# Kernel optimization log

Hardware: AMD Instinct MI355X
Metric: run time of the kernel (lower is better)

The kernel has to match this reference:

```python
import jax, jax.numpy as jnp
import numpy as np


def _conv1d(x, w):
    # x: (B, W, Cin), w: (K, Cin, Cout), SAME padding, stride 1
    return jax.lax.conv_general_dilated(
        x, w, window_strides=(1,), padding='SAME',
        dimension_numbers=('NWC', 'WIO', 'NWC'))


def setup_inputs() -> dict:
    key = jax.random.key(0)
    ks = jax.random.split(key, 5)
    B, T, F, C, K = 64, 64, 256, 64, 9  # batch, num_frames, frame_size(noise_size), filters, kernel
    z = jax.random.normal(ks[0], (B, T, F, 1), dtype=jnp.float32)
    h0 = jax.random.normal(ks[1], (B, F, C), dtype=jnp.float32)
    c0 = jax.random.normal(ks[2], (B, F, C), dtype=jnp.float32)
    Wx = jax.random.normal(ks[3], (K, 1, 4 * C), dtype=jnp.float32) * 0.1
    Wh = jax.random.normal(ks[4], (K, C, 4 * C), dtype=jnp.float32) * 0.1
    b = jnp.zeros((4 * C,), dtype=jnp.float32)
    return {'z': z, 'h0': h0, 'c0': c0, 'Wx': Wx, 'Wh': Wh, 'b': b}


def reference(z, h0, c0, Wx, Wh, b):
    # z: (B, T, F, 1); h0/c0: (B, F, C)
    B = z.shape[0]
    FORGET_BIAS = 1.0  # tf ConvLSTMCell default

    def step(carry, z_t):
        h, c = carry
        gates = _conv1d(z_t, Wx) + _conv1d(h, Wh) + b  # (B, F, 4C)
        i, j, f, o = jnp.split(gates, 4, axis=-1)       # tf gate order: i, new_input, f, o
        c_new = c * jax.nn.sigmoid(f + FORGET_BIAS) + jax.nn.sigmoid(i) * jnp.tanh(j)
        h_new = jnp.tanh(c_new) * jax.nn.sigmoid(o)
        # post_rnn_callback: tanh(mean over channels)
        out = jnp.tanh(jnp.mean(h_new, axis=-1))        # (B, F)
        return (h_new, c_new), out

    z_t_first = jnp.transpose(z, (1, 0, 2, 3))          # (T, B, F, 1)
    (_, _), outs = jax.lax.scan(step, (h0, c0), z_t_first)  # outs: (T, B, F)
    # concat frames along frame axis -> (B, T*F)
    return jnp.transpose(outs, (1, 0, 2)).reshape(B, -1)
```

## Files before the change

kernel.cpp:

```cpp
#include <hip/hip_runtime.h>
#include <hip/hip_bf16.h>

#define BB 64
#define TT 64
#define FF 256
#define CC 64
#define GG 256
#define HP 264
#define GST 264

using frag_ab = __attribute__((ext_vector_type(8))) short;
using f32x4   = __attribute__((ext_vector_type(4))) float;

__device__ __forceinline__ float sigmoidf_(float x) {
    return 1.0f / (1.0f + __expf(-x));
}
__device__ __forceinline__ float tanhf_(float x) {
    const float e = __expf(2.0f * x);
    return 1.0f - 2.0f / (e + 1.0f);
}
__device__ __forceinline__ void split2(float v, short* hi, short* lo) {
    __hip_bfloat16 h = __float2bfloat16(v);
    __hip_bfloat16 l = __float2bfloat16(v - __bfloat162float(h));
    *hi = *reinterpret_cast<short*>(&h);
    *lo = *reinterpret_cast<short*>(&l);
}

__global__ __launch_bounds__(256) void prep_kernel(
    const float* __restrict__ Wh, const float* __restrict__ Wx,
    const float* __restrict__ h0,
    short* __restrict__ WhPh, short* __restrict__ WhPl,
    short* __restrict__ WxTh, short* __restrict__ WxTl,
    short* __restrict__ hAh, short* __restrict__ hAl,
    short* __restrict__ hBh, short* __restrict__ hBl)
{
    const int n = blockIdx.x * 256 + threadIdx.x;
    if (n < BB * HP * CC) {
        const int c = n & 63;
        const int r = (n >> 6) % HP;
        const int b = n / (HP * CC);
        if (r < 4 || r >= 260) {
            hAh[n] = 0; hAl[n] = 0; hBh[n] = 0; hBl[n] = 0;
        } else {
            split2(h0[(b * FF + (r - 4)) * CC + c], &hAh[n], &hAl[n]);
        }
    }
    if (n < 9 * GG * CC) {
        const int c32 = n & 31;
        const int g = (n >> 5) & 255;
        const int p = n >> 13;
        const int k = p >> 1;
        const int cin = (p & 1) * 32 + c32;
        split2(Wh[(k * CC + cin) * GG + g], &WhPh[n], &WhPl[n]);
    }
    if (n < GG * 32) {
        const int kz = n & 31;
        const int g = n >> 5;
        split2(kz < 9 ? Wx[kz * GG + g] : 0.0f, &WxTh[n], &WxTl[n]);
    }
}

__global__ __launch_bounds__(512, 4) void convlstm_step(
    const float* __restrict__ z,
    const short* __restrict__ hinh, const short* __restrict__ hinl,
    const float* __restrict__ c_in,
    const short* __restrict__ WhPh, const short* __restrict__ WhPl,
    const short* __restrict__ WxTh, const short* __restrict__ WxTl,
    const float* __restrict__ bias,
    short* __restrict__ houth, short* __restrict__ houtl,
    float* __restrict__ c_out,
    float* __restrict__ out, int t)
{
    __shared__ __align__(16) char hbyh[72 * 128];
    __shared__ __align__(16) char hbyl[72 * 128];
    __shared__ __align__(16) char zbyh[64 * 64];
    __shared__ __align__(16) char zbyl[64 * 64];
    __shared__ __align__(16) float gbuf[32 * GST];

    const int b = blockIdx.x;
    const int f0 = blockIdx.y * 64;
    const int tid = threadIdx.x;
    const int lane = tid & 63;
    const int w = tid >> 6;

    for (int idx = tid; idx < 72 * 8; idx += 512) {
        const int row = idx >> 3, slot = idx & 7;
        const int off = (b * HP + f0 + row) * CC + slot * 8;
        const frag_ab vh = *reinterpret_cast<const frag_ab*>(hinh + off);
        const frag_ab vl = *reinterpret_cast<const frag_ab*>(hinl + off);
        const int a = row * 128 + ((slot ^ (row & 7)) << 4);
        *reinterpret_cast<frag_ab*>(&hbyh[a]) = vh;
        *reinterpret_cast<frag_ab*>(&hbyl[a]) = vl;
    }
    if (tid < 256) {
        const int row = tid >> 2, slot = tid & 3;
        const float* zr = z + ((long)b * TT + t) * FF;
        short vh[8], vl[8];
        #pragma unroll
        for (int j = 0; j < 8; ++j) {
            const int kz = slot * 8 + j;
            const int f = f0 + row - 4 + kz;
            const float val = (kz < 9 && f >= 0 && f < FF) ? zr[f] : 0.0f;
            split2(val, &vh[j], &vl[j]);
        }
        const int a = row * 64 + ((slot ^ (row & 3)) << 4);
        *reinterpret_cast<frag_ab*>(&zbyh[a]) = *reinterpret_cast<frag_ab*>(vh);
        *reinterpret_cast<frag_ab*>(&zbyl[a]) = *reinterpret_cast<frag_ab*>(vl);
    }
    __syncthreads();

    const int rA = lane & 15;
    const int sA = lane >> 4;
    const int gbase = w * 32;

    f32x4 acc[4][2];
    #pragma unroll
    for (int gtI = 0; gtI < 2; ++gtI) {
        const float bv = bias[gbase + gtI * 16 + rA];
        #pragma unroll
        for (int Mt = 0; Mt < 4; ++Mt) acc[Mt][gtI] = (f32x4){bv, bv, bv, bv};
    }

    const int bln = rA * 32 + sA * 8;
    frag_ab cb[4];
    {
        const int o0 = (0 * GG + gbase) * 32 + bln;
        cb[0] = *reinterpret_cast<const frag_ab*>(WhPh + o0);
        cb[1] = *reinterpret_cast<const frag_ab*>(WhPh + o0 + 16 * 32);
        cb[2] = *reinterpret_cast<const frag_ab*>(WhPl + o0);
        cb[3] = *reinterpret_cast<const frag_ab*>(WhPl + o0 + 16 * 32);
    }

    #pragma unroll
    for (int p = 0; p < 18; ++p) {
        frag_ab nb[4];
        if (p < 17) {
            const int o0 = ((p + 1) * GG + gbase) * 32 + bln;
            nb[0] = *reinterpret_cast<const frag_ab*>(WhPh + o0);
            nb[1] = *reinterpret_cast<const frag_ab*>(WhPh + o0 + 16 * 32);
            nb[2] = *reinterpret_cast<const frag_ab*>(WhPl + o0);
            nb[3] = *reinterpret_cast<const frag_ab*>(WhPl + o0 + 16 * 32);
        } else {
            const int o0 = gbase * 32 + bln;
            nb[0] = *reinterpret_cast<const frag_ab*>(WxTh + o0);
            nb[1] = *reinterpret_cast<const frag_ab*>(WxTh + o0 + 16 * 32);
            nb[2] = *reinterpret_cast<const frag_ab*>(WxTl + o0);
            nb[3] = *reinterpret_cast<const frag_ab*>(WxTl + o0 + 16 * 32);
        }
        const int k = p >> 1, kk = p & 1;
        const int sl = kk * 4 + sA;
        frag_ab ah[4], al[4];
        #pragma unroll
        for (int Mt = 0; Mt < 4; ++Mt) {
            const int r = Mt * 16 + rA + k;
            const int a = r * 128 + ((sl ^ (r & 7)) << 4);
            ah[Mt] = *reinterpret_cast<const frag_ab*>(&hbyh[a]);
            al[Mt] = *reinterpret_cast<const frag_ab*>(&hbyl[a]);
        }
        #pragma unroll
        for (int Mt = 0; Mt < 4; ++Mt) {
            acc[Mt][0] = __builtin_amdgcn_mfma_f32_16x16x32_bf16(ah[Mt], cb[0], acc[Mt][0], 0, 0, 0);
            acc[Mt][1] = __builtin_amdgcn_mfma_f32_16x16x32_bf16(ah[Mt], cb[1], acc[Mt][1], 0, 0, 0);
        }
        #pragma unroll
        for (int Mt = 0; Mt < 4; ++Mt) {
            acc[Mt][0] = __builtin_amdgcn_mfma_f32_16x16x32_bf16(ah[Mt], cb[2], acc[Mt][0], 0, 0, 0);
            acc[Mt][1] = __builtin_amdgcn_mfma_f32_16x16x32_bf16(ah[Mt], cb[3], acc[Mt][1], 0, 0, 0);
        }
        #pragma unroll
        for (int Mt = 0; Mt < 4; ++Mt) {
            acc[Mt][0] = __builtin_amdgcn_mfma_f32_16x16x32_bf16(al[Mt], cb[0], acc[Mt][0], 0, 0, 0);
            acc[Mt][1] = __builtin_amdgcn_mfma_f32_16x16x32_bf16(al[Mt], cb[1], acc[Mt][1], 0, 0, 0);
        }
        cb[0] = nb[0]; cb[1] = nb[1]; cb[2] = nb[2]; cb[3] = nb[3];
    }
    {
        frag_ab ah[4], al[4];
        #pragma unroll
        for (int Mt = 0; Mt < 4; ++Mt) {
            const int r = Mt * 16 + rA;
            const int a = r * 64 + ((sA ^ (r & 3)) << 4);
            ah[Mt] = *reinterpret_cast<const frag_ab*>(&zbyh[a]);
            al[Mt] = *reinterpret_cast<const frag_ab*>(&zbyl[a]);
        }
        #pragma unroll
        for (int Mt = 0; Mt < 4; ++Mt) {
            acc[Mt][0] = __builtin_amdgcn_mfma_f32_16x16x32_bf16(ah[Mt], cb[0], acc[Mt][0], 0, 0, 0);
            acc[Mt][1] = __builtin_amdgcn_mfma_f32_16x16x32_bf16(ah[Mt], cb[1], acc[Mt][1], 0, 0, 0);
            acc[Mt][0] = __builtin_amdgcn_mfma_f32_16x16x32_bf16(ah[Mt], cb[2], acc[Mt][0], 0, 0, 0);
            acc[Mt][1] = __builtin_amdgcn_mfma_f32_16x16x32_bf16(ah[Mt], cb[3], acc[Mt][1], 0, 0, 0);
            acc[Mt][0] = __builtin_amdgcn_mfma_f32_16x16x32_bf16(al[Mt], cb[0], acc[Mt][0], 0, 0, 0);
            acc[Mt][1] = __builtin_amdgcn_mfma_f32_16x16x32_bf16(al[Mt], cb[1], acc[Mt][1], 0, 0, 0);
        }
    }

    #pragma unroll
    for (int pass = 0; pass < 2; ++pass) {
        if (pass) __syncthreads();
        #pragma unroll
        for (int Mh = 0; Mh < 2; ++Mh) {
            const int Mt = pass * 2 + Mh;
            #pragma unroll
            for (int gtI = 0; gtI < 2; ++gtI) {
                const int g = gbase + gtI * 16 + rA;
                float* gp = &gbuf[(Mh * 16 + sA * 4) * GST + g];
                gp[0]       = acc[Mt][gtI][0];
                gp[GST]     = acc[Mt][gtI][1];
                gp[2 * GST] = acc[Mt][gtI][2];
                gp[3 * GST] = acc[Mt][gtI][3];
            }
        }
        __syncthreads();

        const int fl = tid >> 4;
        const int ch0 = (tid & 15) * 4;
        const int frow = pass * 32 + fl;
        const int f = f0 + frow;
        const float* gr = &gbuf[fl * GST];
        const f32x4 gi = *reinterpret_cast<const f32x4*>(gr + ch0);
        const f32x4 gj = *reinterpret_cast<const f32x4*>(gr + 64 + ch0);
        const f32x4 gf = *reinterpret_cast<const f32x4*>(gr + 128 + ch0);
        const f32x4 go = *reinterpret_cast<const f32x4*>(gr + 192 + ch0);

        const int cix = (b * FF + f) * CC + ch0;
        const float4 cold = *reinterpret_cast<const float4*>(&c_in[cix]);
        const float co_[4] = {cold.x, cold.y, cold.z, cold.w};

        float hsum = 0.0f;
        float cv[4];
        short hh[4], hl[4];
        #pragma unroll
        for (int j = 0; j < 4; ++j) {
            const float cnew = co_[j] * sigmoidf_(gf[j] + 1.0f) + sigmoidf_(gi[j]) * tanhf_(gj[j]);
            const float hnew = tanhf_(cnew) * sigmoidf_(go[j]);
            cv[j] = cnew;
            split2(hnew, &hh[j], &hl[j]);
            hsum += hnew;
        }
        *reinterpret_cast<float4*>(&c_out[cix]) = make_float4(cv[0], cv[1], cv[2], cv[3]);
        const int hix = (b * HP + 4 + f) * CC + ch0;
        *reinterpret_cast<uint2*>(&houth[hix]) = *reinterpret_cast<uint2*>(hh);
        *reinterpret_cast<uint2*>(&houtl[hix]) = *reinterpret_cast<uint2*>(hl);

        hsum += __shfl_xor(hsum, 1);
        hsum += __shfl_xor(hsum, 2);
        hsum += __shfl_xor(hsum, 4);
        hsum += __shfl_xor(hsum, 8);
        if ((tid & 15) == 0)
            out[(long)b * (TT * FF) + t * FF + f] = tanhf_(hsum * (1.0f / 64.0f));
    }
}

extern "C" void kernel_launch(void* const* d_in, const int* in_sizes, int n_in,
                              void* d_out, int out_size, void* d_ws, size_t ws_size,
                              hipStream_t stream) {
    const float* z    = (const float*)d_in[0];
    const float* h0   = (const float*)d_in[1];
    const float* c0   = (const float*)d_in[2];
    const float* Wx   = (const float*)d_in[3];
    const float* Wh   = (const float*)d_in[4];
    const float* bias = (const float*)d_in[5];
    float* out = (float*)d_out;

    const int SEp = BB * HP * CC;
    const int SE  = BB * FF * CC;
    short* hAh = (short*)d_ws;
    short* hAl = hAh + SEp;
    short* hBh = hAl + SEp;
    short* hBl = hBh + SEp;
    float* cW  = (float*)(hBl + SEp);
    short* WhPh = (short*)(cW + SE);
    short* WhPl = WhPh + 9 * GG * CC;
    short* WxTh = WhPl + 9 * GG * CC;
    short* WxTl = WxTh + GG * 32;

    prep_kernel<<<(SEp + 255) / 256, 256, 0, stream>>>(Wh, Wx, h0, WhPh, WhPl,
                                                       WxTh, WxTl, hAh, hAl, hBh, hBl);

    dim3 grid(BB, FF / 64);
    for (int t = 0; t < TT; ++t) {
        const short* hih = (t & 1) ? hBh : hAh;
        const short* hil = (t & 1) ? hBl : hAl;
        short* hoh = (t & 1) ? hAh : hBh;
        short* hol = (t & 1) ? hAl : hBl;
        const float* cin = (t == 0) ? c0 : cW;
        convlstm_step<<<grid, 512, 0, stream>>>(z, hih, hil, cin,
                                                WhPh, WhPl, WxTh, WxTl, bias,
                                                hoh, hol, cW, out, t);
    }
}
```

Measured before the change: 1.026 ms.

## Software-pipeline LDS A-fragment loads and prefetch c/bias/weights before staging

Restructures the MFMA main loop so the next iteration's shared-memory h fragments are loaded alongside the next weight fragments, double-buffering both A and B operands. The z-input tile is folded in as a 19th pipeline stage. The first weight fragments, the bias values and the old cell state c are issued before the LDS staging loop so their global latency overlaps with it. MFMA blocks are wrapped in s_setprio, and launch bounds are relaxed from 4 to 2 waves per SIMD so the extra live registers fit. The cost is higher register pressure and possibly lower occupancy.

```diff
diff --git a/kernel.cpp b/kernel.cpp
--- a/kernel.cpp
+++ b/kernel.cpp
@@ -60,7 +60,7 @@
     }
 }
 
-__global__ __launch_bounds__(512, 4) void convlstm_step(
+__global__ __launch_bounds__(512, 2) void convlstm_step(
     const float* __restrict__ z,
     const short* __restrict__ hinh, const short* __restrict__ hinl,
     const float* __restrict__ c_in,
@@ -83,6 +83,28 @@
     const int lane = tid & 63;
     const int w = tid >> 6;
 
+    const int rA = lane & 15;
+    const int sA = lane >> 4;
+    const int gbase = w * 32;
+    const int bln = rA * 32 + sA * 8;
+
+    frag_ab cb[4];
+    {
+        const int o0 = gbase * 32 + bln;
+        cb[0] = *reinterpret_cast<const frag_ab*>(WhPh + o0);
+        cb[1] = *reinterpret_cast<const frag_ab*>(WhPh + o0 + 512);
+        cb[2] = *reinterpret_cast<const frag_ab*>(WhPl + o0);
+        cb[3] = *reinterpret_cast<const frag_ab*>(WhPl + o0 + 512);
+    }
+    const int flE = tid >> 4;
+    const int ch0E = (tid & 15) * 4;
+    const int cixE0 = (b * FF + f0 + flE) * CC + ch0E;
+    const int cixE1 = cixE0 + 32 * CC;
+    const float4 cold0 = *reinterpret_cast<const float4*>(&c_in[cixE0]);
+    const float4 cold1 = *reinterpret_cast<const float4*>(&c_in[cixE1]);
+    const float bv0 = bias[gbase + rA];
+    const float bv1 = bias[gbase + 16 + rA];
+
     for (int idx = tid; idx < 72 * 8; idx += 512) {
         const int row = idx >> 3, slot = idx & 7;
         const int off = (b * HP + f0 + row) * CC + slot * 8;
@@ -109,88 +131,76 @@
     }
     __syncthreads();
 
-    const int rA = lane & 15;
-    const int sA = lane >> 4;
-    const int gbase = w * 32;
-
     f32x4 acc[4][2];
     #pragma unroll
-    for (int gtI = 0; gtI < 2; ++gtI) {
-        const float bv = bias[gbase + gtI * 16 + rA];
-        #pragma unroll
-        for (int Mt = 0; Mt < 4; ++Mt) acc[Mt][gtI] = (f32x4){bv, bv, bv, bv};
-    }
-
-    const int bln = rA * 32 + sA * 8;
-    frag_ab cb[4];
-    {
-        const int o0 = (0 * GG + gbase) * 32 + bln;
-        cb[0] = *reinterpret_cast<const frag_ab*>(WhPh + o0);
-        cb[1] = *reinterpret_cast<const frag_ab*>(WhPh + o0 + 16 * 32);
-        cb[2] = *reinterpret_cast<const frag_ab*>(WhPl + o0);
-        cb[3] = *reinterpret_cast<const frag_ab*>(WhPl + o0 + 16 * 32);
-    }
-
-    #pragma unroll
-    for (int p = 0; p < 18; ++p) {
-        frag_ab nb[4];
+    for (int Mt = 0; Mt < 4; ++Mt) {
+        acc[Mt][0] = (f32x4){bv0, bv0, bv0, bv0};
+        acc[Mt][1] = (f32x4){bv1, bv1, bv1, bv1};
+    }
+
+    frag_ab cah[4], cal[4];
+    #pragma unroll
+    for (int Mt = 0; Mt < 4; ++Mt) {
+        const int r = Mt * 16 + rA;
+        const int a = r * 128 + ((sA ^ (r & 7)) << 4);
+        cah[Mt] = *reinterpret_cast<const frag_ab*>(&hbyh[a]);
+        cal[Mt] = *reinterpret_cast<const frag_ab*>(&hbyl[a]);
+    }
+
+    #pragma unroll
+    for (int p = 0; p < 19; ++p) {
+        frag_ab nah[4], nal[4], nb[4];
         if (p < 17) {
-            const int o0 = ((p + 1) * GG + gbase) * 32 + bln;
+            const int pn = p + 1;
+            const int k = pn >> 1, kk = pn & 1;
+            const int sl = kk * 4 + sA;
+            #pragma unroll
+            for (int Mt = 0; Mt < 4; ++Mt) {
+                const int r = Mt * 16 + rA + k;
+                const int a = r * 128 + ((sl ^ (r & 7)) << 4);
+                nah[Mt] = *reinterpret_cast<const frag_ab*>(&hbyh[a]);
+                nal[Mt] = *reinterpret_cast<const frag_ab*>(&hbyl[a]);
+            }
+            const int o0 = (pn * GG + gbase) * 32 + bln;
             nb[0] = *reinterpret_cast<const frag_ab*>(WhPh + o0);
-            nb[1] = *reinterpret_cast<const frag_ab*>(WhPh + o0 + 16 * 32);
+            nb[1] = *reinterpret_cast<const frag_ab*>(WhPh + o0 + 512);
             nb[2] = *reinterpret_cast<const frag_ab*>(WhPl + o0);
-            nb[3] = *reinterpret_cast<const frag_ab*>(WhPl + o0 + 16 * 32);
-        } else {
+            nb[3] = *reinterpret_cast<const frag_ab*>(WhPl + o0 + 512);
+        } else if (p == 17) {
+            #pragma unroll
+            for (int Mt = 0; Mt < 4; ++Mt) {
+                const int r = Mt * 16 + rA;
+                const int a = r * 64 + ((sA ^ (r & 3)) << 4);
+                nah[Mt] = *reinterpret_cast<const frag_ab*>(&zbyh[a]);
+                nal[Mt] = *reinterpret_cast<const frag_ab*>(&zbyl[a]);
+            }
             const int o0 = gbase * 32 + bln;
             nb[0] = *reinterpret_cast<const frag_ab*>(WxTh + o0);
-            nb[1] = *reinterpret_cast<const frag_ab*>(WxTh + o0 + 16 * 32);
+            nb[1] = *reinterpret_cast<const frag_ab*>(WxTh + o0 + 512);
             nb[2] = *reinterpret_cast<const frag_ab*>(WxTl + o0);
-            nb[3] = *reinterpret_cast<const frag_ab*>(WxTl + o0 + 16 * 32);
-        }
-        const int k = p >> 1, kk = p & 1;
-        const int sl = kk * 4 + sA;
-        frag_ab ah[4], al[4];
+            nb[3] = *reinterpret_cast<const frag_ab*>(WxTl + o0 + 512);
+        }
+        __builtin_amdgcn_s_setprio(1);
         #pragma unroll
         for (int Mt = 0; Mt < 4; ++Mt) {
-            const int r = Mt * 16 + rA + k;
-            const int a = r * 128 + ((sl ^ (r & 7)) << 4);
-            ah[Mt] = *reinterpret_cast<const frag_ab*>(&hbyh[a]);
-            al[Mt] = *reinterpret_cast<const frag_ab*>(&hbyl[a]);
+            acc[Mt][0] = __builtin_amdgcn_mfma_f32_16x16x32_bf16(cah[Mt], cb[0], acc[Mt][0], 0, 0, 0);
+            acc[Mt][1] = __builtin_amdgcn_mfma_f32_16x16x32_bf16(cah[Mt], cb[1], acc[Mt][1], 0, 0, 0);
         }
         #pragma unroll
         for (int Mt = 0; Mt < 4; ++Mt) {
-            acc[Mt][0] = __builtin_amdgcn_mfma_f32_16x16x32_bf16(ah[Mt], cb[0], acc[Mt][0], 0, 0, 0);
-            acc[Mt][1] = __builtin_amdgcn_mfma_f32_16x16x32_bf16(ah[Mt], cb[1], acc[Mt][1], 0, 0, 0);
+            acc[Mt][0] = __builtin_amdgcn_mfma_f32_16x16x32_bf16(cah[Mt], cb[2], acc[Mt][0], 0, 0, 0);
+            acc[Mt][1] = __builtin_amdgcn_mfma_f32_16x16x32_bf16(cah[Mt], cb[3], acc[Mt][1], 0, 0, 0);
         }
         #pragma unroll
         for (int Mt = 0; Mt < 4; ++Mt) {
-            acc[Mt][0] = __builtin_amdgcn_mfma_f32_16x16x32_bf16(ah[Mt], cb[2], acc[Mt][0], 0, 0, 0);
-            acc[Mt][1] = __builtin_amdgcn_mfma_f32_16x16x32_bf16(ah[Mt], cb[3], acc[Mt][1], 0, 0, 0);
-        }
-        #pragma unroll
-        for (int Mt = 0; Mt < 4; ++Mt) {
-            acc[Mt][0] = __builtin_amdgcn_mfma_f32_16x16x32_bf16(al[Mt], cb[0], acc[Mt][0], 0, 0, 0);
-            acc[Mt][1] = __builtin_amdgcn_mfma_f32_16x16x32_bf16(al[Mt], cb[1], acc[Mt][1], 0, 0, 0);
-        }
-        cb[0] = nb[0]; cb[1] = nb[1]; cb[2] = nb[2]; cb[3] = nb[3];
-    }
-    {
-        frag_ab ah[4], al[4];
-        #pragma unroll
-        for (int Mt = 0; Mt < 4; ++Mt) {
-            const int r = Mt * 16 + rA;
-            const int a = r * 64 + ((sA ^ (r & 3)) << 4);
-            ah[Mt] = *reinterpret_cast<const frag_ab*>(&zbyh[a]);
-            al[Mt] = *reinterpret_cast<const frag_ab*>(&zbyl[a]);
-        }
-        #pragma unroll
-        for (int Mt = 0; Mt < 4; ++Mt) {
-            acc[Mt][0] = __builtin_amdgcn_mfma_f32_16x16x32_bf16(ah[Mt], cb[0], acc[Mt][0], 0, 0, 0);
-            acc[Mt][1] = __builtin_amdgcn_mfma_f32_16x16x32_bf16(ah[Mt], cb[1], acc[Mt][1], 0, 0, 0);
-            acc[Mt][0] = __builtin_amdgcn_mfma_f32_16x16x32_bf16(ah[Mt], cb[2], acc[Mt][0], 0, 0, 0);
-            acc[Mt][1] = __builtin_amdgcn_mfma_f32_16x16x32_bf16(ah[Mt], cb[3], acc[Mt][1], 0, 0, 0);
-            acc[Mt][0] = __builtin_amdgcn_mfma_f32_16x16x32_bf16(al[Mt], cb[0], acc[Mt][0], 0, 0, 0);
-            acc[Mt][1] = __builtin_amdgcn_mfma_f32_16x16x32_bf16(al[Mt], cb[1], acc[Mt][1], 0, 0, 0);
+            acc[Mt][0] = __builtin_amdgcn_mfma_f32_16x16x32_bf16(cal[Mt], cb[0], acc[Mt][0], 0, 0, 0);
+            acc[Mt][1] = __builtin_amdgcn_mfma_f32_16x16x32_bf16(cal[Mt], cb[1], acc[Mt][1], 0, 0, 0);
+        }
+        __builtin_amdgcn_s_setprio(0);
+        if (p < 18) {
+            #pragma unroll
+            for (int Mt = 0; Mt < 4; ++Mt) { cah[Mt] = nah[Mt]; cal[Mt] = nal[Mt]; }
+            cb[0] = nb[0]; cb[1] = nb[1]; cb[2] = nb[2]; cb[3] = nb[3];
         }
     }
 
@@ -212,18 +222,14 @@
         }
         __syncthreads();
 
-        const int fl = tid >> 4;
-        const int ch0 = (tid & 15) * 4;
-        const int frow = pass * 32 + fl;
-        const int f = f0 + frow;
-        const float* gr = &gbuf[fl * GST];
-        const f32x4 gi = *reinterpret_cast<const f32x4*>(gr + ch0);
-        const f32x4 gj = *reinterpret_cast<const f32x4*>(gr + 64 + ch0);
-        const f32x4 gf = *reinterpret_cast<const f32x4*>(gr + 128 + ch0);
-        const f32x4 go = *reinterpret_cast<const f32x4*>(gr + 192 + ch0);
-
-        const int cix = (b * FF + f) * CC + ch0;
-        const float4 cold = *reinterpret_cast<const float4*>(&c_in[cix]);
+        const int f = f0 + pass * 32 + flE;
+        const float* gr = &gbuf[flE * GST];
+        const f32x4 gi = *reinterpret_cast<const f32x4*>(gr + ch0E);
+        const f32x4 gj = *reinterpret_cast<const f32x4*>(gr + 64 + ch0E);
+        const f32x4 gf = *reinterpret_cast<const f32x4*>(gr + 128 + ch0E);
+        const f32x4 go = *reinterpret_cast<const f32x4*>(gr + 192 + ch0E);
+
+        const float4 cold = pass ? cold1 : cold0;
         const float co_[4] = {cold.x, cold.y, cold.z, cold.w};
 
         float hsum = 0.0f;
@@ -237,8 +243,9 @@
             split2(hnew, &hh[j], &hl[j]);
             hsum += hnew;
         }
+        const int cix = (b * FF + f) * CC + ch0E;
         *reinterpret_cast<float4*>(&c_out[cix]) = make_float4(cv[0], cv[1], cv[2], cv[3]);
-        const int hix = (b * HP + 4 + f) * CC + ch0;
+        const int hix = (b * HP + 4 + f) * CC + ch0E;
         *reinterpret_cast<uint2*>(&houth[hix]) = *reinterpret_cast<uint2*>(hh);
         *reinterpret_cast<uint2*>(&houtl[hix]) = *reinterpret_cast<uint2*>(hl);
 
```

Result: no change. 1.029 ms (+0.3%).

## Retile ConvLSTM step to 32-frame blocks with 256 threads and wider gate tiles

Applied to the files above, without the earlier changes.

Halves the frame tile per block (64 to 32) and threads (512 to 256), so the grid doubles to 512 blocks, and each wave now covers 64 gate columns over 2 M tiles instead of 32 columns over 4. The weight fragment loads are restructured per gate tile, c_in and bias loads are hoisted before the h staging, the z-projection is folded into the main loop, and s_setprio wraps the MFMA bursts. The epilogue becomes a single pass with 8 channels per thread, removing the second gbuf round-trip and a barrier. This aims for more parallelism per timestep and less serialization, at the cost of redundant halo loads (40 rows per 32) and more weight-fragment traffic per output.

```diff
diff --git a/kernel.cpp b/kernel.cpp
--- a/kernel.cpp
+++ b/kernel.cpp
@@ -7,7 +7,8 @@
 #define CC 64
 #define GG 256
 #define HP 264
-#define GST 264
+#define TFR 32
+#define GST 260
 
 using frag_ab = __attribute__((ext_vector_type(8))) short;
 using f32x4   = __attribute__((ext_vector_type(4))) float;
@@ -60,7 +61,7 @@
     }
 }
 
-__global__ __launch_bounds__(512, 4) void convlstm_step(
+__global__ __launch_bounds__(256, 2) void convlstm_step(
     const float* __restrict__ z,
     const short* __restrict__ hinh, const short* __restrict__ hinl,
     const float* __restrict__ c_in,
@@ -71,19 +72,41 @@
     float* __restrict__ c_out,
     float* __restrict__ out, int t)
 {
-    __shared__ __align__(16) char hbyh[72 * 128];
-    __shared__ __align__(16) char hbyl[72 * 128];
-    __shared__ __align__(16) char zbyh[64 * 64];
-    __shared__ __align__(16) char zbyl[64 * 64];
-    __shared__ __align__(16) float gbuf[32 * GST];
+    __shared__ __align__(16) char hbyh[40 * 128];
+    __shared__ __align__(16) char hbyl[40 * 128];
+    __shared__ __align__(16) char zbyh[32 * 64];
+    __shared__ __align__(16) char zbyl[32 * 64];
+    __shared__ __align__(16) float gbuf[TFR * GST];
 
     const int b = blockIdx.x;
-    const int f0 = blockIdx.y * 64;
+    const int f0 = blockIdx.y * TFR;
     const int tid = threadIdx.x;
     const int lane = tid & 63;
     const int w = tid >> 6;
 
-    for (int idx = tid; idx < 72 * 8; idx += 512) {
+    const int rA = lane & 15;
+    const int sA = lane >> 4;
+    const int gbase = w * 64;
+    const int bln = rA * 32 + sA * 8;
+
+    frag_ab cbh[4], cbl[4];
+    #pragma unroll
+    for (int gtI = 0; gtI < 4; ++gtI) {
+        const int o0 = (gbase + gtI * 16 + rA) * 32 + sA * 8;
+        cbh[gtI] = *reinterpret_cast<const frag_ab*>(WhPh + o0);
+        cbl[gtI] = *reinterpret_cast<const frag_ab*>(WhPl + o0);
+    }
+    const int flE = tid >> 3;
+    const int ch0E = (tid & 7) * 8;
+    const int cixE = (b * FF + f0 + flE) * CC + ch0E;
+    const float4 cold0 = *reinterpret_cast<const float4*>(&c_in[cixE]);
+    const float4 cold1 = *reinterpret_cast<const float4*>(&c_in[cixE + 4]);
+
+    float bv[4];
+    #pragma unroll
+    for (int gtI = 0; gtI < 4; ++gtI) bv[gtI] = bias[gbase + gtI * 16 + rA];
+
+    for (int idx = tid; idx < 40 * 8; idx += 256) {
         const int row = idx >> 3, slot = idx & 7;
         const int off = (b * HP + f0 + row) * CC + slot * 8;
         const frag_ab vh = *reinterpret_cast<const frag_ab*>(hinh + off);
@@ -92,7 +115,7 @@
         *reinterpret_cast<frag_ab*>(&hbyh[a]) = vh;
         *reinterpret_cast<frag_ab*>(&hbyl[a]) = vl;
     }
-    if (tid < 256) {
+    if (tid < 128) {
         const int row = tid >> 2, slot = tid & 3;
         const float* zr = z + ((long)b * TT + t) * FF;
         short vh[8], vl[8];
@@ -109,146 +132,117 @@
     }
     __syncthreads();
 
-    const int rA = lane & 15;
-    const int sA = lane >> 4;
-    const int gbase = w * 32;
-
-    f32x4 acc[4][2];
-    #pragma unroll
-    for (int gtI = 0; gtI < 2; ++gtI) {
-        const float bv = bias[gbase + gtI * 16 + rA];
-        #pragma unroll
-        for (int Mt = 0; Mt < 4; ++Mt) acc[Mt][gtI] = (f32x4){bv, bv, bv, bv};
-    }
-
-    const int bln = rA * 32 + sA * 8;
-    frag_ab cb[4];
-    {
-        const int o0 = (0 * GG + gbase) * 32 + bln;
-        cb[0] = *reinterpret_cast<const frag_ab*>(WhPh + o0);
-        cb[1] = *reinterpret_cast<const frag_ab*>(WhPh + o0 + 16 * 32);
-        cb[2] = *reinterpret_cast<const frag_ab*>(WhPl + o0);
-        cb[3] = *reinterpret_cast<const frag_ab*>(WhPl + o0 + 16 * 32);
-    }
-
-    #pragma unroll
-    for (int p = 0; p < 18; ++p) {
-        frag_ab nb[4];
+    f32x4 acc[2][4];
+    #pragma unroll
+    for (int Mt = 0; Mt < 2; ++Mt)
+        #pragma unroll
+        for (int gtI = 0; gtI < 4; ++gtI)
+            acc[Mt][gtI] = (f32x4){bv[gtI], bv[gtI], bv[gtI], bv[gtI]};
+
+    #pragma unroll
+    for (int p = 0; p < 19; ++p) {
+        frag_ab nbh[4], nbl[4];
         if (p < 17) {
-            const int o0 = ((p + 1) * GG + gbase) * 32 + bln;
-            nb[0] = *reinterpret_cast<const frag_ab*>(WhPh + o0);
-            nb[1] = *reinterpret_cast<const frag_ab*>(WhPh + o0 + 16 * 32);
-            nb[2] = *reinterpret_cast<const frag_ab*>(WhPl + o0);
-            nb[3] = *reinterpret_cast<const frag_ab*>(WhPl + o0 + 16 * 32);
+            #pragma unroll
+            for (int gtI = 0; gtI < 4; ++gtI) {
+                const int o0 = ((p + 1) * GG + gbase + gtI * 16 + rA) * 32 + sA * 8;
+                nbh[gtI] = *reinterpret_cast<const frag_ab*>(WhPh + o0);
+                nbl[gtI] = *reinterpret_cast<const frag_ab*>(WhPl + o0);
+            }
+        } else if (p == 17) {
+            #pragma unroll
+            for (int gtI = 0; gtI < 4; ++gtI) {
+                const int o0 = (gbase + gtI * 16 + rA) * 32 + sA * 8;
+                nbh[gtI] = *reinterpret_cast<const frag_ab*>(WxTh + o0);
+                nbl[gtI] = *reinterpret_cast<const frag_ab*>(WxTl + o0);
+            }
+        }
+        frag_ab ah[2], al[2];
+        if (p < 18) {
+            const int k = p >> 1, kk = p & 1;
+            const int sl = kk * 4 + sA;
+            #pragma unroll
+            for (int Mt = 0; Mt < 2; ++Mt) {
+                const int r = Mt * 16 + rA + k;
+                const int a = r * 128 + ((sl ^ (r & 7)) << 4);
+                ah[Mt] = *reinterpret_cast<const frag_ab*>(&hbyh[a]);
+                al[Mt] = *reinterpret_cast<const frag_ab*>(&hbyl[a]);
+            }
         } else {
-            const int o0 = gbase * 32 + bln;
-            nb[0] = *reinterpret_cast<const frag_ab*>(WxTh + o0);
-            nb[1] = *reinterpret_cast<const frag_ab*>(WxTh + o0 + 16 * 32);
-            nb[2] = *reinterpret_cast<const frag_ab*>(WxTl + o0);
-            nb[3] = *reinterpret_cast<const frag_ab*>(WxTl + o0 + 16 * 32);
-        }
-        const int k = p >> 1, kk = p & 1;
-        const int sl = kk * 4 + sA;
-        frag_ab ah[4], al[4];
-        #pragma unroll
-        for (int Mt = 0; Mt < 4; ++Mt) {
-            const int r = Mt * 16 + rA + k;
-            const int a = r * 128 + ((sl ^ (r & 7)) << 4);
-            ah[Mt] = *reinterpret_cast<const frag_ab*>(&hbyh[a]);
-            al[Mt] = *reinterpret_cast<const frag_ab*>(&hbyl[a]);
-        }
-        #pragma unroll
-        for (int Mt = 0; Mt < 4; ++Mt) {
-            acc[Mt][0] = __builtin_amdgcn_mfma_f32_16x16x32_bf16(ah[Mt], cb[0], acc[Mt][0], 0, 0, 0);
-            acc[Mt][1] = __builtin_amdgcn_mfma_f32_16x16x32_bf16(ah[Mt], cb[1], acc[Mt][1], 0, 0, 0);
-        }
-        #pragma unroll
-        for (int Mt = 0; Mt < 4; ++Mt) {
-            acc[Mt][0] = __builtin_amdgcn_mfma_f32_16x16x32_bf16(ah[Mt], cb[2], acc[Mt][0], 0, 0, 0);
-            acc[Mt][1] = __builtin_amdgcn_mfma_f32_16x16x32_bf16(ah[Mt], cb[3], acc[Mt][1], 0, 0, 0);
-        }
-        #pragma unroll
-        for (int Mt = 0; Mt < 4; ++Mt) {
-            acc[Mt][0] = __builtin_amdgcn_mfma_f32_16x16x32_bf16(al[Mt], cb[0], acc[Mt][0], 0, 0, 0);
-            acc[Mt][1] = __builtin_amdgcn_mfma_f32_16x16x32_bf16(al[Mt], cb[1], acc[Mt][1], 0, 0, 0);
-        }
-        cb[0] = nb[0]; cb[1] = nb[1]; cb[2] = nb[2]; cb[3] = nb[3];
-    }
-    {
-        frag_ab ah[4], al[4];
-        #pragma unroll
-        for (int Mt = 0; Mt < 4; ++Mt) {
-            const int r = Mt * 16 + rA;
-            const int a = r * 64 + ((sA ^ (r & 3)) << 4);
-            ah[Mt] = *reinterpret_cast<const frag_ab*>(&zbyh[a]);
-            al[Mt] = *reinterpret_cast<const frag_ab*>(&zbyl[a]);
-        }
-        #pragma unroll
-        for (int Mt = 0; Mt < 4; ++Mt) {
-            acc[Mt][0] = __builtin_amdgcn_mfma_f32_16x16x32_bf16(ah[Mt], cb[0], acc[Mt][0], 0, 0, 0);
-            acc[Mt][1] = __builtin_amdgcn_mfma_f32_16x16x32_bf16(ah[Mt], cb[1], acc[Mt][1], 0, 0, 0);
-            acc[Mt][0] = __builtin_amdgcn_mfma_f32_16x16x32_bf16(ah[Mt], cb[2], acc[Mt][0], 0, 0, 0);
-            acc[Mt][1] = __builtin_amdgcn_mfma_f32_16x16x32_bf16(ah[Mt], cb[3], acc[Mt][1], 0, 0, 0);
-            acc[Mt][0] = __builtin_amdgcn_mfma_f32_16x16x32_bf16(al[Mt], cb[0], acc[Mt][0], 0, 0, 0);
-            acc[Mt][1] = __builtin_amdgcn_mfma_f32_16x16x32_bf16(al[Mt], cb[1], acc[Mt][1], 0, 0, 0);
-        }
-    }
-
-    #pragma unroll
-    for (int pass = 0; pass < 2; ++pass) {
-        if (pass) __syncthreads();
-        #pragma unroll
-        for (int Mh = 0; Mh < 2; ++Mh) {
-            const int Mt = pass * 2 + Mh;
-            #pragma unroll
-            for (int gtI = 0; gtI < 2; ++gtI) {
-                const int g = gbase + gtI * 16 + rA;
-                float* gp = &gbuf[(Mh * 16 + sA * 4) * GST + g];
-                gp[0]       = acc[Mt][gtI][0];
-                gp[GST]     = acc[Mt][gtI][1];
-                gp[2 * GST] = acc[Mt][gtI][2];
-                gp[3 * GST] = acc[Mt][gtI][3];
-            }
-        }
-        __syncthreads();
-
-        const int fl = tid >> 4;
-        const int ch0 = (tid & 15) * 4;
-        const int frow = pass * 32 + fl;
-        const int f = f0 + frow;
-        const float* gr = &gbuf[fl * GST];
-        const f32x4 gi = *reinterpret_cast<const f32x4*>(gr + ch0);
-        const f32x4 gj = *reinterpret_cast<const f32x4*>(gr + 64 + ch0);
-        const f32x4 gf = *reinterpret_cast<const f32x4*>(gr + 128 + ch0);
-        const f32x4 go = *reinterpret_cast<const f32x4*>(gr + 192 + ch0);
-
-        const int cix = (b * FF + f) * CC + ch0;
-        const float4 cold = *reinterpret_cast<const float4*>(&c_in[cix]);
-        const float co_[4] = {cold.x, cold.y, cold.z, cold.w};
-
-        float hsum = 0.0f;
-        float cv[4];
-        short hh[4], hl[4];
-        #pragma unroll
-        for (int j = 0; j < 4; ++j) {
-            const float cnew = co_[j] * sigmoidf_(gf[j] + 1.0f) + sigmoidf_(gi[j]) * tanhf_(gj[j]);
-            const float hnew = tanhf_(cnew) * sigmoidf_(go[j]);
-            cv[j] = cnew;
-            split2(hnew, &hh[j], &hl[j]);
-            hsum += hnew;
-        }
-        *reinterpret_cast<float4*>(&c_out[cix]) = make_float4(cv[0], cv[1], cv[2], cv[3]);
-        const int hix = (b * HP + 4 + f) * CC + ch0;
-        *reinterpret_cast<uint2*>(&houth[hix]) = *reinterpret_cast<uint2*>(hh);
-        *reinterpret_cast<uint2*>(&houtl[hix]) = *reinterpret_cast<uint2*>(hl);
-
-        hsum += __shfl_xor(hsum, 1);
-        hsum += __shfl_xor(hsum, 2);
-        hsum += __shfl_xor(hsum, 4);
-        hsum += __shfl_xor(hsum, 8);
-        if ((tid & 15) == 0)
-            out[(long)b * (TT * FF) + t * FF + f] = tanhf_(hsum * (1.0f / 64.0f));
-    }
+            #pragma unroll
+            for (int Mt = 0; Mt < 2; ++Mt) {
+                const int r = Mt * 16 + rA;
+                const int a = r * 64 + ((sA ^ (r & 3)) << 4);
+                ah[Mt] = *reinterpret_cast<const frag_ab*>(&zbyh[a]);
+                al[Mt] = *reinterpret_cast<const frag_ab*>(&zbyl[a]);
+            }
+        }
+        __builtin_amdgcn_s_setprio(1);
+        #pragma unroll
+        for (int gtI = 0; gtI < 4; ++gtI) {
+            #pragma unroll
+            for (int Mt = 0; Mt < 2; ++Mt) {
+                acc[Mt][gtI] = __builtin_amdgcn_mfma_f32_16x16x32_bf16(ah[Mt], cbh[gtI], acc[Mt][gtI], 0, 0, 0);
+                acc[Mt][gtI] = __builtin_amdgcn_mfma_f32_16x16x32_bf16(ah[Mt], cbl[gtI], acc[Mt][gtI], 0, 0, 0);
+                acc[Mt][gtI] = __builtin_amdgcn_mfma_f32_16x16x32_bf16(al[Mt], cbh[gtI], acc[Mt][gtI], 0, 0, 0);
+            }
+        }
+        __builtin_amdgcn_s_setprio(0);
+        if (p < 18) {
+            #pragma unroll
+            for (int gtI = 0; gtI < 4; ++gtI) { cbh[gtI] = nbh[gtI]; cbl[gtI] = nbl[gtI]; }
+        }
+    }
+
+    #pragma unroll
+    for (int Mt = 0; Mt < 2; ++Mt)
+        #pragma unroll
+        for (int gtI = 0; gtI < 4; ++gtI) {
+            float* gp = &gbuf[(Mt * 16 + sA * 4) * GST + gbase + gtI * 16 + rA];
+            gp[0]       = acc[Mt][gtI][0];
+            gp[GST]     = acc[Mt][gtI][1];
+            gp[2 * GST] = acc[Mt][gtI][2];
+            gp[3 * GST] = acc[Mt][gtI][3];
+        }
+    __syncthreads();
+
+    const float* gr = &gbuf[flE * GST];
+    const f32x4 gia = *reinterpret_cast<const f32x4*>(gr + ch0E);
+    const f32x4 gib = *reinterpret_cast<const f32x4*>(gr + ch0E + 4);
+    const f32x4 gja = *reinterpret_cast<const f32x4*>(gr + 64 + ch0E);
+    const f32x4 gjb = *reinterpret_cast<const f32x4*>(gr + 64 + ch0E + 4);
+    const f32x4 gfa = *reinterpret_cast<const f32x4*>(gr + 128 + ch0E);
+    const f32x4 gfb = *reinterpret_cast<const f32x4*>(gr + 128 + ch0E + 4);
+    const f32x4 goa = *reinterpret_cast<const f32x4*>(gr + 192 + ch0E);
+    const f32x4 gob = *reinterpret_cast<const f32x4*>(gr + 192 + ch0E + 4);
+    const float gi[8] = {gia[0], gia[1], gia[2], gia[3], gib[0], gib[1], gib[2], gib[3]};
+    const float gj[8] = {gja[0], gja[1], gja[2], gja[3], gjb[0], gjb[1], gjb[2], gjb[3]};
+    const float gf[8] = {gfa[0], gfa[1], gfa[2], gfa[3], gfb[0], gfb[1], gfb[2], gfb[3]};
+    const float go[8] = {goa[0], goa[1], goa[2], goa[3], gob[0], gob[1], gob[2], gob[3]};
+    const float co_[8] = {cold0.x, cold0.y, cold0.z, cold0.w, cold1.x, cold1.y, cold1.z, cold1.w};
+
+    float hsum = 0.0f;
+    float cv[8];
+    short hh[8], hl[8];
+    #pragma unroll
+    for (int j = 0; j < 8; ++j) {
+        const float cnew = co_[j] * sigmoidf_(gf[j] + 1.0f) + sigmoidf_(gi[j]) * tanhf_(gj[j]);
+        const float hnew = tanhf_(cnew) * sigmoidf_(go[j]);
+        cv[j] = cnew;
+        split2(hnew, &hh[j], &hl[j]);
+        hsum += hnew;
+    }
+    *reinterpret_cast<float4*>(&c_out[cixE])     = make_float4(cv[0], cv[1], cv[2], cv[3]);
+    *reinterpret_cast<float4*>(&c_out[cixE + 4]) = make_float4(cv[4], cv[5], cv[6], cv[7]);
+    const int hix = (b * HP + 4 + f0 + flE) * CC + ch0E;
+    *reinterpret_cast<frag_ab*>(&houth[hix]) = *reinterpret_cast<frag_ab*>(hh);
+    *reinterpret_cast<frag_ab*>(&houtl[hix]) = *reinterpret_cast<frag_ab*>(hl);
+
+    hsum += __shfl_xor(hsum, 1);
+    hsum += __shfl_xor(hsum, 2);
+    hsum += __shfl_xor(hsum, 4);
+    if ((tid & 7) == 0)
+        out[(long)b * (TT * FF) + t * FF + f0 + flE] = tanhf_(hsum * (1.0f / 64.0f));
 }
 
 extern "C" void kernel_launch(void* const* d_in, const int* in_sizes, int n_in,
@@ -277,14 +271,14 @@
     prep_kernel<<<(SEp + 255) / 256, 256, 0, stream>>>(Wh, Wx, h0, WhPh, WhPl,
                                                        WxTh, WxTl, hAh, hAl, hBh, hBl);
 
-    dim3 grid(BB, FF / 64);
+    dim3 grid(BB, FF / TFR);
     for (int t = 0; t < TT; ++t) {
         const short* hih = (t & 1) ? hBh : hAh;
         const short* hil = (t & 1) ? hBl : hAl;
         short* hoh = (t & 1) ? hAh : hBh;
         short* hol = (t & 1) ? hAl : hBl;
         const float* cin = (t == 0) ? c0 : cW;
-        convlstm_step<<<grid, 512, 0, stream>>>(z, hih, hil, cin,
+        convlstm_step<<<grid, 256, 0, stream>>>(z, hih, hil, cin,
                                                 WhPh, WhPl, WxTh, WxTl, bias,
                                                 hoh, hol, cW, out, t);
     }
```

Measured after the change: 1.397 ms. 36.2% more time.

## Split gate channels across blocks and defer mean-tanh output to next step

Applied to the files above, without the earlier changes.

Adds a third grid dimension that splits the 256 gate columns into four channel groups of 64, so each block runs 128 threads instead of 512 and the grid has four times as many blocks. The weights are permuted so that each channel group's i/j/f/o gates land next to each other, which lets each block apply the LSTM pointwise update without seeing the other groups. Because no block holds all channels any more, the per-frame mean over channels is computed from the stored h at the start of the next step, plus a final kernel for the last frame. It also prefetches weights, bias and old c before the barrier and adds setprio around the MFMA bursts. In exchange, every block reloads the same h tile and z window (redundant global and LDS traffic), and the output is reduced from the bf16 hi/lo split of h rather than from full fp32 h.

```diff
diff --git a/kernel.cpp b/kernel.cpp
--- a/kernel.cpp
+++ b/kernel.cpp
@@ -7,7 +7,7 @@
 #define CC 64
 #define GG 256
 #define HP 264
-#define GST 264
+#define GSTE 68
 
 using frag_ab = __attribute__((ext_vector_type(8))) short;
 using f32x4   = __attribute__((ext_vector_type(4))) float;
@@ -24,6 +24,9 @@
     __hip_bfloat16 l = __float2bfloat16(v - __bfloat162float(h));
     *hi = *reinterpret_cast<short*>(&h);
     *lo = *reinterpret_cast<short*>(&l);
+}
+__device__ __forceinline__ float bf2f(short s) {
+    return __uint_as_float(((unsigned)(unsigned short)s) << 16);
 }
 
 __global__ __launch_bounds__(256) void prep_kernel(
@@ -47,20 +50,44 @@
     }
     if (n < 9 * GG * CC) {
         const int c32 = n & 31;
-        const int g = (n >> 5) & 255;
+        const int gp = (n >> 5) & 255;
         const int p = n >> 13;
         const int k = p >> 1;
         const int cin = (p & 1) * 32 + c32;
+        const int g = (gp & 3) * 64 + (gp >> 2);
         split2(Wh[(k * CC + cin) * GG + g], &WhPh[n], &WhPl[n]);
     }
     if (n < GG * 32) {
         const int kz = n & 31;
-        const int g = n >> 5;
+        const int gp = n >> 5;
+        const int g = (gp & 3) * 64 + (gp >> 2);
         split2(kz < 9 ? Wx[kz * GG + g] : 0.0f, &WxTh[n], &WxTl[n]);
     }
 }
 
-__global__ __launch_bounds__(512, 4) void convlstm_step(
+__global__ __launch_bounds__(128) void finalize_out(
+    const short* __restrict__ hh, const short* __restrict__ hl,
+    float* __restrict__ out)
+{
+    const int b = blockIdx.x;
+    const int f0 = blockIdx.y * 64;
+    const int tid = threadIdx.x;
+    const int fl = tid >> 1, part = tid & 1;
+    const long hb = ((long)(b * HP + 4 + f0 + fl)) * CC + part * 32;
+    float s = 0.0f;
+    #pragma unroll
+    for (int q = 0; q < 4; ++q) {
+        const frag_ab vh = *reinterpret_cast<const frag_ab*>(hh + hb + q * 8);
+        const frag_ab vl = *reinterpret_cast<const frag_ab*>(hl + hb + q * 8);
+        #pragma unroll
+        for (int j = 0; j < 8; ++j) s += bf2f(vh[j]) + bf2f(vl[j]);
+    }
+    s += __shfl_xor(s, 1);
+    if (part == 0)
+        out[(long)b * (TT * FF) + (TT - 1) * FF + f0 + fl] = tanhf_(s * (1.0f / 64.0f));
+}
+
+__global__ __launch_bounds__(128, 2) void convlstm_step(
     const float* __restrict__ z,
     const short* __restrict__ hinh, const short* __restrict__ hinl,
     const float* __restrict__ c_in,
@@ -75,15 +102,41 @@
     __shared__ __align__(16) char hbyl[72 * 128];
     __shared__ __align__(16) char zbyh[64 * 64];
     __shared__ __align__(16) char zbyl[64 * 64];
-    __shared__ __align__(16) float gbuf[32 * GST];
+    __shared__ __align__(16) float gbuf[32 * GSTE];
 
     const int b = blockIdx.x;
     const int f0 = blockIdx.y * 64;
+    const int cg = blockIdx.z;
     const int tid = threadIdx.x;
     const int lane = tid & 63;
     const int w = tid >> 6;
 
-    for (int idx = tid; idx < 72 * 8; idx += 512) {
+    const int rA = lane & 15;
+    const int sA = lane >> 4;
+    const int gbase = cg * 64 + w * 32;
+
+    frag_ab cb[4];
+    {
+        const int o0 = (gbase + rA) * 32 + sA * 8;
+        cb[0] = *reinterpret_cast<const frag_ab*>(WhPh + o0);
+        cb[1] = *reinterpret_cast<const frag_ab*>(WhPh + o0 + 512);
+        cb[2] = *reinterpret_cast<const frag_ab*>(WhPl + o0);
+        cb[3] = *reinterpret_cast<const frag_ab*>(WhPl + o0 + 512);
+    }
+    float bv[2];
+    #pragma unroll
+    for (int gtI = 0; gtI < 2; ++gtI) {
+        const int gq = gbase + gtI * 16 + rA;
+        bv[gtI] = bias[((gq & 3) << 6) + (gq >> 2)];
+    }
+    const int flE = tid >> 2;
+    const int ch0E = cg * 16 + (tid & 3) * 4;
+    const int cix0 = (b * FF + f0 + flE) * CC + ch0E;
+    const int cix1 = cix0 + 32 * CC;
+    const float4 cold0 = *reinterpret_cast<const float4*>(&c_in[cix0]);
+    const float4 cold1 = *reinterpret_cast<const float4*>(&c_in[cix1]);
+
+    for (int idx = tid; idx < 72 * 8; idx += 128) {
         const int row = idx >> 3, slot = idx & 7;
         const int off = (b * HP + f0 + row) * CC + slot * 8;
         const frag_ab vh = *reinterpret_cast<const frag_ab*>(hinh + off);
@@ -92,8 +145,8 @@
         *reinterpret_cast<frag_ab*>(&hbyh[a]) = vh;
         *reinterpret_cast<frag_ab*>(&hbyl[a]) = vl;
     }
-    if (tid < 256) {
-        const int row = tid >> 2, slot = tid & 3;
+    for (int idx = tid; idx < 256; idx += 128) {
+        const int row = idx >> 2, slot = idx & 3;
         const float* zr = z + ((long)b * TT + t) * FF;
         short vh[8], vl[8];
         #pragma unroll
@@ -107,56 +160,67 @@
         *reinterpret_cast<frag_ab*>(&zbyh[a]) = *reinterpret_cast<frag_ab*>(vh);
         *reinterpret_cast<frag_ab*>(&zbyl[a]) = *reinterpret_cast<frag_ab*>(vl);
     }
+    if (cg == 0 && t > 0) {
+        const int fl = tid >> 1, part = tid & 1;
+        const long hb = ((long)(b * HP + 4 + f0 + fl)) * CC + part * 32;
+        float s = 0.0f;
+        #pragma unroll
+        for (int q = 0; q < 4; ++q) {
+            const frag_ab vh = *reinterpret_cast<const frag_ab*>(hinh + hb + q * 8);
+            const frag_ab vl = *reinterpret_cast<const frag_ab*>(hinl + hb + q * 8);
+            #pragma unroll
+            for (int j = 0; j < 8; ++j) s += bf2f(vh[j]) + bf2f(vl[j]);
+        }
+        s += __shfl_xor(s, 1);
+        if (part == 0)
+            out[(long)b * (TT * FF) + (t - 1) * FF + f0 + fl] = tanhf_(s * (1.0f / 64.0f));
+    }
     __syncthreads();
 
-    const int rA = lane & 15;
-    const int sA = lane >> 4;
-    const int gbase = w * 32;
-
     f32x4 acc[4][2];
     #pragma unroll
-    for (int gtI = 0; gtI < 2; ++gtI) {
-        const float bv = bias[gbase + gtI * 16 + rA];
-        #pragma unroll
-        for (int Mt = 0; Mt < 4; ++Mt) acc[Mt][gtI] = (f32x4){bv, bv, bv, bv};
-    }
-
-    const int bln = rA * 32 + sA * 8;
-    frag_ab cb[4];
-    {
-        const int o0 = (0 * GG + gbase) * 32 + bln;
-        cb[0] = *reinterpret_cast<const frag_ab*>(WhPh + o0);
-        cb[1] = *reinterpret_cast<const frag_ab*>(WhPh + o0 + 16 * 32);
-        cb[2] = *reinterpret_cast<const frag_ab*>(WhPl + o0);
-        cb[3] = *reinterpret_cast<const frag_ab*>(WhPl + o0 + 16 * 32);
-    }
-
-    #pragma unroll
-    for (int p = 0; p < 18; ++p) {
+    for (int Mt = 0; Mt < 4; ++Mt) {
+        acc[Mt][0] = (f32x4){bv[0], bv[0], bv[0], bv[0]};
+        acc[Mt][1] = (f32x4){bv[1], bv[1], bv[1], bv[1]};
+    }
+
+    #pragma unroll
+    for (int p = 0; p < 19; ++p) {
         frag_ab nb[4];
         if (p < 17) {
-            const int o0 = ((p + 1) * GG + gbase) * 32 + bln;
+            const int o0 = ((p + 1) * GG + gbase + rA) * 32 + sA * 8;
             nb[0] = *reinterpret_cast<const frag_ab*>(WhPh + o0);
-            nb[1] = *reinterpret_cast<const frag_ab*>(WhPh + o0 + 16 * 32);
+            nb[1] = *reinterpret_cast<const frag_ab*>(WhPh + o0 + 512);
             nb[2] = *reinterpret_cast<const frag_ab*>(WhPl + o0);
-            nb[3] = *reinterpret_cast<const frag_ab*>(WhPl + o0 + 16 * 32);
+            nb[3] = *reinterpret_cast<const frag_ab*>(WhPl + o0 + 512);
+        } else if (p == 17) {
+            const int o0 = (gbase + rA) * 32 + sA * 8;
+            nb[0] = *reinterpret_cast<const frag_ab*>(WxTh + o0);
+            nb[1] = *reinterpret_cast<const frag_ab*>(WxTh + o0 + 512);
+            nb[2] = *reinterpret_cast<const frag_ab*>(WxTl + o0);
+            nb[3] = *reinterpret_cast<const frag_ab*>(WxTl + o0 + 512);
+        }
+        frag_ab ah[4], al[4];
+        if (p < 18) {
+            const int k = p >> 1, kk = p & 1;
+            const int sl = kk * 4 + sA;
+            #pragma unroll
+            for (int Mt = 0; Mt < 4; ++Mt) {
+                const int r = Mt * 16 + rA + k;
+                const int a = r * 128 + ((sl ^ (r & 7)) << 4);
+                ah[Mt] = *reinterpret_cast<const frag_ab*>(&hbyh[a]);
+                al[Mt] = *reinterpret_cast<const frag_ab*>(&hbyl[a]);
+            }
         } else {
-            const int o0 = gbase * 32 + bln;
-            nb[0] = *reinterpret_cast<const frag_ab*>(WxTh + o0);
-            nb[1] = *reinterpret_cast<const frag_ab*>(WxTh + o0 + 16 * 32);
-            nb[2] = *reinterpret_cast<const frag_ab*>(WxTl + o0);
-            nb[3] = *reinterpret_cast<const frag_ab*>(WxTl + o0 + 16 * 32);
-        }
-        const int k = p >> 1, kk = p & 1;
-        const int sl = kk * 4 + sA;
-        frag_ab ah[4], al[4];
-        #pragma unroll
-        for (int Mt = 0; Mt < 4; ++Mt) {
-            const int r = Mt * 16 + rA + k;
-            const int a = r * 128 + ((sl ^ (r & 7)) << 4);
-            ah[Mt] = *reinterpret_cast<const frag_ab*>(&hbyh[a]);
-            al[Mt] = *reinterpret_cast<const frag_ab*>(&hbyl[a]);
-        }
+            #pragma unroll
+            for (int Mt = 0; Mt < 4; ++Mt) {
+                const int r = Mt * 16 + rA;
+                const int a = r * 64 + ((sA ^ (r & 3)) << 4);
+                ah[Mt] = *reinterpret_cast<const frag_ab*>(&zbyh[a]);
+                al[Mt] = *reinterpret_cast<const frag_ab*>(&zbyl[a]);
+            }
+        }
+        __builtin_amdgcn_s_setprio(1);
         #pragma unroll
         for (int Mt = 0; Mt < 4; ++Mt) {
             acc[Mt][0] = __builtin_amdgcn_mfma_f32_16x16x32_bf16(ah[Mt], cb[0], acc[Mt][0], 0, 0, 0);
@@ -172,26 +236,8 @@
             acc[Mt][0] = __builtin_amdgcn_mfma_f32_16x16x32_bf16(al[Mt], cb[0], acc[Mt][0], 0, 0, 0);
             acc[Mt][1] = __builtin_amdgcn_mfma_f32_16x16x32_bf16(al[Mt], cb[1], acc[Mt][1], 0, 0, 0);
         }
-        cb[0] = nb[0]; cb[1] = nb[1]; cb[2] = nb[2]; cb[3] = nb[3];
-    }
-    {
-        frag_ab ah[4], al[4];
-        #pragma unroll
-        for (int Mt = 0; Mt < 4; ++Mt) {
-            const int r = Mt * 16 + rA;
-            const int a = r * 64 + ((sA ^ (r & 3)) << 4);
-            ah[Mt] = *reinterpret_cast<const frag_ab*>(&zbyh[a]);
-            al[Mt] = *reinterpret_cast<const frag_ab*>(&zbyl[a]);
-        }
-        #pragma unroll
-        for (int Mt = 0; Mt < 4; ++Mt) {
-            acc[Mt][0] = __builtin_amdgcn_mfma_f32_16x16x32_bf16(ah[Mt], cb[0], acc[Mt][0], 0, 0, 0);
-            acc[Mt][1] = __builtin_amdgcn_mfma_f32_16x16x32_bf16(ah[Mt], cb[1], acc[Mt][1], 0, 0, 0);
-            acc[Mt][0] = __builtin_amdgcn_mfma_f32_16x16x32_bf16(ah[Mt], cb[2], acc[Mt][0], 0, 0, 0);
-            acc[Mt][1] = __builtin_amdgcn_mfma_f32_16x16x32_bf16(ah[Mt], cb[3], acc[Mt][1], 0, 0, 0);
-            acc[Mt][0] = __builtin_amdgcn_mfma_f32_16x16x32_bf16(al[Mt], cb[0], acc[Mt][0], 0, 0, 0);
-            acc[Mt][1] = __builtin_amdgcn_mfma_f32_16x16x32_bf16(al[Mt], cb[1], acc[Mt][1], 0, 0, 0);
-        }
+        __builtin_amdgcn_s_setprio(0);
+        if (p < 18) { cb[0] = nb[0]; cb[1] = nb[1]; cb[2] = nb[2]; cb[3] = nb[3]; }
     }
 
     #pragma unroll
@@ -202,52 +248,39 @@
             const int Mt = pass * 2 + Mh;
             #pragma unroll
             for (int gtI = 0; gtI < 2; ++gtI) {
-                const int g = gbase + gtI * 16 + rA;
-                float* gp = &gbuf[(Mh * 16 + sA * 4) * GST + g];
-                gp[0]       = acc[Mt][gtI][0];
-                gp[GST]     = acc[Mt][gtI][1];
-                gp[2 * GST] = acc[Mt][gtI][2];
-                gp[3 * GST] = acc[Mt][gtI][3];
+                float* gp = &gbuf[(Mh * 16 + sA * 4) * GSTE + w * 32 + gtI * 16 + rA];
+                gp[0]        = acc[Mt][gtI][0];
+                gp[GSTE]     = acc[Mt][gtI][1];
+                gp[2 * GSTE] = acc[Mt][gtI][2];
+                gp[3 * GSTE] = acc[Mt][gtI][3];
             }
         }
         __syncthreads();
 
-        const int fl = tid >> 4;
-        const int ch0 = (tid & 15) * 4;
-        const int frow = pass * 32 + fl;
-        const int f = f0 + frow;
-        const float* gr = &gbuf[fl * GST];
-        const f32x4 gi = *reinterpret_cast<const f32x4*>(gr + ch0);
-        const f32x4 gj = *reinterpret_cast<const f32x4*>(gr + 64 + ch0);
-        const f32x4 gf = *reinterpret_cast<const f32x4*>(gr + 128 + ch0);
-        const f32x4 go = *reinterpret_cast<const f32x4*>(gr + 192 + ch0);
-
-        const int cix = (b * FF + f) * CC + ch0;
-        const float4 cold = *reinterpret_cast<const float4*>(&c_in[cix]);
+        const int f = f0 + pass * 32 + flE;
+        const float* gr = &gbuf[flE * GSTE + (tid & 3) * 16];
+        const f32x4 v0 = *reinterpret_cast<const f32x4*>(gr);
+        const f32x4 v1 = *reinterpret_cast<const f32x4*>(gr + 4);
+        const f32x4 v2 = *reinterpret_cast<const f32x4*>(gr + 8);
+        const f32x4 v3 = *reinterpret_cast<const f32x4*>(gr + 12);
+        const float4 cold = pass ? cold1 : cold0;
         const float co_[4] = {cold.x, cold.y, cold.z, cold.w};
 
-        float hsum = 0.0f;
         float cv[4];
         short hh[4], hl[4];
         #pragma unroll
         for (int j = 0; j < 4; ++j) {
-            const float cnew = co_[j] * sigmoidf_(gf[j] + 1.0f) + sigmoidf_(gi[j]) * tanhf_(gj[j]);
-            const float hnew = tanhf_(cnew) * sigmoidf_(go[j]);
+            const f32x4 g = (j == 0) ? v0 : (j == 1) ? v1 : (j == 2) ? v2 : v3;
+            const float cnew = co_[j] * sigmoidf_(g[2] + 1.0f) + sigmoidf_(g[0]) * tanhf_(g[1]);
+            const float hnew = tanhf_(cnew) * sigmoidf_(g[3]);
             cv[j] = cnew;
             split2(hnew, &hh[j], &hl[j]);
-            hsum += hnew;
-        }
+        }
+        const int cix = (b * FF + f) * CC + ch0E;
         *reinterpret_cast<float4*>(&c_out[cix]) = make_float4(cv[0], cv[1], cv[2], cv[3]);
-        const int hix = (b * HP + 4 + f) * CC + ch0;
+        const int hix = (b * HP + 4 + f) * CC + ch0E;
         *reinterpret_cast<uint2*>(&houth[hix]) = *reinterpret_cast<uint2*>(hh);
         *reinterpret_cast<uint2*>(&houtl[hix]) = *reinterpret_cast<uint2*>(hl);
-
-        hsum += __shfl_xor(hsum, 1);
-        hsum += __shfl_xor(hsum, 2);
-        hsum += __shfl_xor(hsum, 4);
-        hsum += __shfl_xor(hsum, 8);
-        if ((tid & 15) == 0)
-            out[(long)b * (TT * FF) + t * FF + f] = tanhf_(hsum * (1.0f / 64.0f));
     }
 }
 
@@ -277,15 +310,16 @@
     prep_kernel<<<(SEp + 255) / 256, 256, 0, stream>>>(Wh, Wx, h0, WhPh, WhPl,
                                                        WxTh, WxTl, hAh, hAl, hBh, hBl);
 
-    dim3 grid(BB, FF / 64);
+    dim3 grid(BB, FF / 64, 4);
     for (int t = 0; t < TT; ++t) {
         const short* hih = (t & 1) ? hBh : hAh;
         const short* hil = (t & 1) ? hBl : hAl;
         short* hoh = (t & 1) ? hAh : hBh;
         short* hol = (t & 1) ? hAl : hBl;
         const float* cin = (t == 0) ? c0 : cW;
-        convlstm_step<<<grid, 512, 0, stream>>>(z, hih, hil, cin,
+        convlstm_step<<<grid, 128, 0, stream>>>(z, hih, hil, cin,
                                                 WhPh, WhPl, WxTh, WxTl, bias,
                                                 hoh, hol, cW, out, t);
     }
-}
+    finalize_out<<<dim3(BB, FF / 64), 128, 0, stream>>>(hAh, hAl, out);
+}
```

Result: slower. 1.066 ms (+3.9%).
